# Optimization experiments

Measured on AMD Instinct MI355X. Metric: run time of the kernel, lower is better.

## Reference

```python
import jax, jax.numpy as jnp
import numpy as np

S, R, C, H, D = 128, 384, 256, 8, 32  # N_seq, N_res, C_m, heads, head_dim
INF = 1e9
EPS = 1e-5


def _layernorm(x, w, b):
    mu = jnp.mean(x, axis=-1, keepdims=True)
    var = jnp.mean(jnp.square(x - mu), axis=-1, keepdims=True)
    return (x - mu) * jax.lax.rsqrt(var + EPS) * w + b


def setup_inputs() -> dict:
    key = jax.random.key(0)
    ks = jax.random.split(key, 8)
    sc = 0.02
    m = jax.random.normal(ks[0], (S, R, C), jnp.float32)
    mask = jnp.ones((S, R), jnp.float32)
    ln_w = jnp.ones((C,), jnp.float32)
    ln_b = jnp.zeros((C,), jnp.float32)
    wq = jax.random.normal(ks[1], (C, H * D), jnp.float32) * sc
    wk = jax.random.normal(ks[2], (C, H * D), jnp.float32) * sc
    wv = jax.random.normal(ks[3], (C, H * D), jnp.float32) * sc
    wg = jax.random.normal(ks[4], (C, H * D), jnp.float32) * sc
    bg = jnp.ones((H * D,), jnp.float32)  # gate bias init to 1 (openfold convention)
    wo = jax.random.normal(ks[5], (H * D, C), jnp.float32) * sc
    bo = jnp.zeros((C,), jnp.float32)
    return {"m": m, "mask": mask, "ln_w": ln_w, "ln_b": ln_b,
            "wq": wq, "wk": wk, "wv": wv, "wg": wg, "bg": bg,
            "wo": wo, "bo": bo}


def reference(m, mask, ln_w, ln_b, wq, wk, wv, wg, bg, wo, bo):
    # mask bias: [S, 1, 1, R], 0 where mask==1, -inf-ish where mask==0
    mask_bias = (INF * (mask - 1.0))[:, None, None, :]
    x = _layernorm(m, ln_w, ln_b)                        # [S, R, C]
    q = (x @ wq).reshape(S, R, H, D) * (D ** -0.5)       # [S, R, H, D]
    k = (x @ wk).reshape(S, R, H, D)
    v = (x @ wv).reshape(S, R, H, D)
    scores = jnp.einsum('sqhd,skhd->shqk', q, k) + mask_bias  # [S, H, R, R]
    a = jax.nn.softmax(scores, axis=-1)
    o = jnp.einsum('shqk,skhd->sqhd', a, v)              # [S, R, H, D]
    g = jax.nn.sigmoid(x @ wg + bg).reshape(S, R, H, D)  # gate
    o = (o * g).reshape(S, R, H * D)
    return o @ wo + bo                                   # [S, R, C]
```

## Files before the change

kernel.cpp:

```cpp
#include <hip/hip_runtime.h>
#include <cstdint>
#include <cstddef>

#define S_  128
#define R_  384
#define C_  256
#define H_  8
#define D_  32
#define HD_ 256
#define M_  (S_*R_)

#define LOG2E 1.4426950408889634f

typedef float f32x16 __attribute__((ext_vector_type(16)));
typedef short s16x8  __attribute__((ext_vector_type(8)));
typedef int   i32x4  __attribute__((ext_vector_type(4)));

__device__ __forceinline__ unsigned short f2bf(float f) {
  uint32_t u = __float_as_uint(f);
  u += 0x7fffu + ((u >> 16) & 1u);
  return (unsigned short)(u >> 16);
}
__device__ __forceinline__ float bf2f(unsigned short s) {
  return __uint_as_float(((uint32_t)s) << 16);
}
__device__ __forceinline__ uint32_t pkbf(float lo, float hi) {
  return (uint32_t)f2bf(lo) | ((uint32_t)f2bf(hi) << 16);
}
#define MFMA32(a,b,c) __builtin_amdgcn_mfma_f32_32x32x16_bf16((a),(b),(c),0,0,0)

__device__ __forceinline__ void gload16(const void* g, void* l) {
  __builtin_amdgcn_global_load_lds(
      (const __attribute__((address_space(1))) void*)g,
      (__attribute__((address_space(3))) void*)l, 16, 0, 0);
}

__global__ __launch_bounds__(256) void prep_w(const float* __restrict__ wq,
    const float* __restrict__ wk, const float* __restrict__ wv,
    const float* __restrict__ wg, const float* __restrict__ wo,
    unsigned short* __restrict__ WT) {
  __shared__ unsigned short Tl[64][72];
  const int mat = blockIdx.x >> 4;
  const int t   = blockIdx.x & 15;
  const int k0  = (t >> 2) * 64, n0 = (t & 3) * 64;
  const float* W = (mat==0)?wq:(mat==1)?wk:(mat==2)?wv:(mat==3)?wg:wo;
  const int tx = threadIdx.x & 63, ty = threadIdx.x >> 6;
#pragma unroll
  for (int i = 0; i < 16; i++) {
    int kk = ty + i * 4;
    Tl[tx][kk] = f2bf(W[(size_t)(k0 + kk) * 256 + n0 + tx]);
  }
  __syncthreads();
#pragma unroll
  for (int i = 0; i < 16; i++) {
    int nn = ty + i * 4;
    WT[(size_t)mat * 65536 + (size_t)(n0 + nn) * 256 + k0 + tx] = Tl[nn][tx];
  }
}

__global__ __launch_bounds__(256) void ln_kernel(const float* __restrict__ mIn,
    const float* __restrict__ w, const float* __restrict__ b,
    unsigned short* __restrict__ x) {
  int row  = blockIdx.x * 4 + (threadIdx.x >> 6);
  int lane = threadIdx.x & 63;
  const float4 v4 = *(const float4*)(mIn + (size_t)row * C_ + lane * 4);
  float s  = v4.x + v4.y + v4.z + v4.w;
  float ss = v4.x*v4.x + v4.y*v4.y + v4.z*v4.z + v4.w*v4.w;
#pragma unroll
  for (int off = 32; off > 0; off >>= 1) {
    s  += __shfl_xor(s,  off);
    ss += __shfl_xor(ss, off);
  }
  float mu  = s * (1.0f / C_);
  float var = ss * (1.0f / C_) - mu * mu;
  float rs  = rsqrtf(var + 1e-5f);
  const float4 wv = *(const float4*)(w + lane * 4);
  const float4 bv = *(const float4*)(b + lane * 4);
  uint2 o2;
  o2.x = pkbf((v4.x - mu) * rs * wv.x + bv.x, (v4.y - mu) * rs * wv.y + bv.y);
  o2.y = pkbf((v4.z - mu) * rs * wv.z + bv.z, (v4.w - mu) * rs * wv.w + bv.w);
  *(uint2*)(x + (size_t)row * C_ + lane * 4) = o2;
}

__global__ __launch_bounds__(256, 5) void proj_gemm(const unsigned short* __restrict__ X,
    const unsigned short* __restrict__ WT, const float* __restrict__ bg,
    unsigned short* __restrict__ Qo, unsigned short* __restrict__ Ko,
    unsigned short* __restrict__ Vo, unsigned short* __restrict__ Go) {
  __shared__ __align__(16) unsigned short As[64 * 32];
  __shared__ __align__(16) unsigned short Bs[128 * 32];
  const int tid = threadIdx.x;
  const int wi  = blockIdx.x >> 1;
  const int bn  = (blockIdx.x & 1) * 128;
  const int bm  = blockIdx.y * 64;
  const unsigned short* Wt = WT + (size_t)wi * 65536;
  unsigned short* O = (wi==0)?Qo:(wi==1)?Ko:(wi==2)?Vo:Go;

  const int lane = tid & 63, wid = tid >> 6;
  const int wr = (wid >> 1) * 32, wc = (wid & 1) * 64;
  const int lr = lane & 31, hi = lane >> 5;
  const int srow = lane >> 2, scol = (lane & 3) * 8;

  f32x16 acc0, acc1;
#pragma unroll
  for (int r = 0; r < 16; r++) { acc0[r] = 0.f; acc1[r] = 0.f; }

  for (int k0 = 0; k0 < 256; k0 += 32) {
    gload16(X + (size_t)(bm + wid*16 + srow) * 256 + k0 + scol, &As[wid * 512]);
#pragma unroll
    for (int i = 0; i < 2; i++) {
      const int rb = wid * 32 + i * 16;
      gload16(Wt + (size_t)(bn + rb + srow) * 256 + k0 + scol, &Bs[rb * 32]);
    }
    asm volatile("s_waitcnt vmcnt(0)" ::: "memory");
    __syncthreads();
#pragma unroll
    for (int kh = 0; kh < 2; kh++) {
      s16x8 a0 = *(const s16x8*)&As[(wr + lr) * 32      + kh*16 + 8*hi];
      s16x8 b0 = *(const s16x8*)&Bs[(wc + lr) * 32      + kh*16 + 8*hi];
      s16x8 b1 = *(const s16x8*)&Bs[(wc + 32 + lr) * 32 + kh*16 + 8*hi];
      acc0 = MFMA32(a0, b0, acc0);
      acc1 = MFMA32(a0, b1, acc1);
    }
    __syncthreads();
  }

  const float qs2 = 0.17677669529663687f * LOG2E;
#pragma unroll
  for (int ns = 0; ns < 2; ns++) {
    const f32x16& a = ns ? acc1 : acc0;
    int colg = bn + wc + ns*32 + lr;
    float bgv = (wi == 3) ? bg[colg] : 0.f;
#pragma unroll
    for (int r = 0; r < 16; r++) {
      float v = a[r];
      if (wi == 0) v *= qs2;
      if (wi == 3) v = 1.0f / (1.0f + __expf(-(v + bgv)));
      int row = bm + wr + (r & 3) + 8*(r >> 2) + 4*hi;
      O[(size_t)row * 256 + colg] = f2bf(v);
    }
  }
}

__global__ __launch_bounds__(768, 6) void attn_kernel(const unsigned short* __restrict__ Qb,
    const unsigned short* __restrict__ Kb, const unsigned short* __restrict__ Vb,
    const unsigned short* __restrict__ Gb, const float* __restrict__ mask,
    unsigned short* __restrict__ Ob) {
  __shared__ unsigned short Kl[384][40];
  __shared__ unsigned short VT[32][392];
  __shared__ float mb[384];
  __shared__ float sAl[12][32];

  const int h = blockIdx.x, s = blockIdx.y;
  const int tid = threadIdx.x;
  const int wid = tid >> 6, lane = tid & 63;
  const int lr = lane & 31, hi = lane >> 5;

  if (tid < 384) {
    const unsigned short* ksrc = Kb + ((size_t)(s*R_ + tid)) * 256 + h*32;
    uint4 k0 = *(const uint4*)ksrc;
    uint4 k1 = *(const uint4*)(ksrc + 8);
    uint4 k2 = *(const uint4*)(ksrc + 16);
    uint4 k3 = *(const uint4*)(ksrc + 24);
    *(uint4*)&Kl[tid][0]  = k0;
    *(uint4*)&Kl[tid][8]  = k1;
    *(uint4*)&Kl[tid][16] = k2;
    *(uint4*)&Kl[tid][24] = k3;
    mb[tid] = (1e9f * LOG2E) * (mask[s * R_ + tid] - 1.0f);
  } else {
    const int r = tid - 384;
    const unsigned short* vsrc = Vb + ((size_t)(s*R_ + r)) * 256 + h*32;
    unsigned short tmp[32];
    *(uint4*)(tmp)      = *(const uint4*)vsrc;
    *(uint4*)(tmp + 8)  = *(const uint4*)(vsrc + 8);
    *(uint4*)(tmp + 16) = *(const uint4*)(vsrc + 16);
    *(uint4*)(tmp + 24) = *(const uint4*)(vsrc + 24);
#pragma unroll
    for (int j = 0; j < 32; j++) VT[j][r] = tmp[j];
  }

  const int q0 = wid * 32;
  const unsigned short* qsrc = Qb + ((size_t)(s*R_ + q0 + lr)) * 256 + h*32;
  s16x8 bq0 = *(const s16x8*)(qsrc + 8*hi);
  s16x8 bq1 = *(const s16x8*)(qsrc + 16 + 8*hi);

  f32x16 of;
#pragma unroll
  for (int r = 0; r < 16; r++) of[r] = 0.f;
  float mrun = -1e30f, lsum = 0.f;

  __syncthreads();

  for (int kt = 0; kt < 12; kt++) {
    s16x8 ak0 = *(const s16x8*)&Kl[kt*32 + lr][8*hi];
    s16x8 ak1 = *(const s16x8*)&Kl[kt*32 + lr][16 + 8*hi];
    s16x8 bv0 = *(const s16x8*)&VT[lr][kt*32 + 8*hi];
    s16x8 bv1 = *(const s16x8*)&VT[lr][kt*32 + 16 + 8*hi];

    f32x16 p;
#pragma unroll
    for (int r = 0; r < 16; r++) p[r] = mb[kt*32 + (r & 3) + 8*(r >> 2) + 4*hi];
    __builtin_amdgcn_s_setprio(1);
    p = MFMA32(ak0, bq0, p);
    p = MFMA32(ak1, bq1, p);
    __builtin_amdgcn_s_setprio(0);

    float m01 = fmaxf(fmaxf(p[0], p[1]), fmaxf(p[2], p[3]));
    float m23 = fmaxf(fmaxf(p[4], p[5]), fmaxf(p[6], p[7]));
    float m45 = fmaxf(fmaxf(p[8], p[9]), fmaxf(p[10], p[11]));
    float m67 = fmaxf(fmaxf(p[12], p[13]), fmaxf(p[14], p[15]));
    float pm = fmaxf(fmaxf(m01, m23), fmaxf(m45, m67));
    pm = fmaxf(pm, __shfl_xor(pm, 32));
    if (!__all(pm <= mrun + 11.54f)) {
      float nm = fmaxf(mrun, pm);
      float al = __builtin_amdgcn_exp2f(mrun - nm);
      mrun = nm;
      lsum *= al;
      if (hi == 0) sAl[wid][lr] = al;
#pragma unroll
      for (int r = 0; r < 16; r++)
        of[r] *= sAl[wid][(r & 3) + 8*(r >> 2) + 4*hi];
    }
    float ls = 0.f;
#pragma unroll
    for (int r = 0; r < 16; r++) {
      p[r] = __builtin_amdgcn_exp2f(p[r] - mrun);
      ls += p[r];
    }
    lsum += ls;

    uint32_t w0, w1, w2, w3, w4, w5, w6, w7;
    asm("v_cvt_pk_bf16_f32 %0, %1, %2" : "=v"(w0) : "v"(p[0]),  "v"(p[1]));
    asm("v_cvt_pk_bf16_f32 %0, %1, %2" : "=v"(w1) : "v"(p[2]),  "v"(p[3]));
    asm("v_cvt_pk_bf16_f32 %0, %1, %2" : "=v"(w2) : "v"(p[4]),  "v"(p[5]));
    asm("v_cvt_pk_bf16_f32 %0, %1, %2" : "=v"(w3) : "v"(p[6]),  "v"(p[7]));
    asm("v_cvt_pk_bf16_f32 %0, %1, %2" : "=v"(w4) : "v"(p[8]),  "v"(p[9]));
    asm("v_cvt_pk_bf16_f32 %0, %1, %2" : "=v"(w5) : "v"(p[10]), "v"(p[11]));
    asm("v_cvt_pk_bf16_f32 %0, %1, %2" : "=v"(w6) : "v"(p[12]), "v"(p[13]));
    asm("v_cvt_pk_bf16_f32 %0, %1, %2" : "=v"(w7) : "v"(p[14]), "v"(p[15]));
    asm volatile("v_permlane32_swap_b32 %0, %1" : "+v"(w0), "+v"(w2));
    asm volatile("v_permlane32_swap_b32 %0, %1" : "+v"(w1), "+v"(w3));
    asm volatile("v_permlane32_swap_b32 %0, %1" : "+v"(w4), "+v"(w6));
    asm volatile("v_permlane32_swap_b32 %0, %1" : "+v"(w5), "+v"(w7));
    i32x4 pa0i = {(int)w0, (int)w1, (int)w2, (int)w3};
    i32x4 pa1i = {(int)w4, (int)w5, (int)w6, (int)w7};
    __builtin_amdgcn_s_setprio(1);
    of = MFMA32(__builtin_bit_cast(s16x8, pa0i), bv0, of);
    of = MFMA32(__builtin_bit_cast(s16x8, pa1i), bv1, of);
    __builtin_amdgcn_s_setprio(0);
  }

  float lt = lsum + __shfl_xor(lsum, 32);
  float inv = 1.0f / lt;
  if (hi == 0) sAl[wid][lr] = inv;
#pragma unroll
  for (int r = 0; r < 16; r++) {
    int crow = (r & 3) + 8*(r >> 2) + 4*hi;
    float iv = sAl[wid][crow];
    size_t off = ((size_t)(s*R_ + q0 + crow)) * 256 + h*32 + lr;
    float gv = bf2f(Gb[off]);
    Ob[off] = f2bf(of[r] * iv * gv);
  }
}

__global__ __launch_bounds__(256, 5) void out_gemm(const unsigned short* __restrict__ Ob,
    const unsigned short* __restrict__ WT, const float* __restrict__ bo,
    float* __restrict__ Out) {
  __shared__ __align__(16) unsigned short As[64 * 32];
  __shared__ __align__(16) unsigned short Bs[128 * 32];
  const unsigned short* Wt = WT + 4 * 65536;
  const int tid = threadIdx.x;
  const int bn = blockIdx.x * 128;
  const int bm = blockIdx.y * 64;
  const int lane = tid & 63, wid = tid >> 6;
  const int wr = (wid >> 1) * 32, wc = (wid & 1) * 64;
  const int lr = lane & 31, hi = lane >> 5;
  const int srow = lane >> 2, scol = (lane & 3) * 8;

  f32x16 acc0, acc1;
#pragma unroll
  for (int r = 0; r < 16; r++) { acc0[r] = 0.f; acc1[r] = 0.f; }

  for (int k0 = 0; k0 < 256; k0 += 32) {
    gload16(Ob + (size_t)(bm + wid*16 + srow) * 256 + k0 + scol, &As[wid * 512]);
#pragma unroll
    for (int i = 0; i < 2; i++) {
      const int rb = wid * 32 + i * 16;
      gload16(Wt + (size_t)(bn + rb + srow) * 256 + k0 + scol, &Bs[rb * 32]);
    }
    asm volatile("s_waitcnt vmcnt(0)" ::: "memory");
    __syncthreads();
#pragma unroll
    for (int kh = 0; kh < 2; kh++) {
      s16x8 a0 = *(const s16x8*)&As[(wr + lr) * 32      + kh*16 + 8*hi];
      s16x8 b0 = *(const s16x8*)&Bs[(wc + lr) * 32      + kh*16 + 8*hi];
      s16x8 b1 = *(const s16x8*)&Bs[(wc + 32 + lr) * 32 + kh*16 + 8*hi];
      acc0 = MFMA32(a0, b0, acc0);
      acc1 = MFMA32(a0, b1, acc1);
    }
    __syncthreads();
  }

#pragma unroll
  for (int ns = 0; ns < 2; ns++) {
    const f32x16& a = ns ? acc1 : acc0;
    int colg = bn + wc + ns*32 + lr;
    float bov = bo[colg];
#pragma unroll
    for (int r = 0; r < 16; r++) {
      int row = bm + wr + (r & 3) + 8*(r >> 2) + 4*hi;
      Out[(size_t)row * 256 + colg] = a[r] + bov;
    }
  }
}

extern "C" void kernel_launch(void* const* d_in, const int* in_sizes, int n_in,
                              void* d_out, int out_size, void* d_ws, size_t ws_size,
                              hipStream_t stream) {
  const float* m    = (const float*)d_in[0];
  const float* mask = (const float*)d_in[1];
  const float* ln_w = (const float*)d_in[2];
  const float* ln_b = (const float*)d_in[3];
  const float* wq   = (const float*)d_in[4];
  const float* wk   = (const float*)d_in[5];
  const float* wv   = (const float*)d_in[6];
  const float* wg   = (const float*)d_in[7];
  const float* bg   = (const float*)d_in[8];
  const float* wo   = (const float*)d_in[9];
  const float* bo   = (const float*)d_in[10];
  float* out = (float*)d_out;

  unsigned short* ws = (unsigned short*)d_ws;
  const size_t SZ = (size_t)M_ * 256;
  unsigned short* xbf = ws;
  unsigned short* qb  = ws + 1 * SZ;
  unsigned short* kb  = ws + 2 * SZ;
  unsigned short* vb  = ws + 3 * SZ;
  unsigned short* gb  = ws + 4 * SZ;
  unsigned short* ob  = ws + 5 * SZ;
  unsigned short* WT  = ws + 6 * SZ;

  prep_w<<<80, 256, 0, stream>>>(wq, wk, wv, wg, wo, WT);
  ln_kernel<<<M_ / 4, 256, 0, stream>>>(m, ln_w, ln_b, xbf);
  proj_gemm<<<dim3(8, M_ / 64), 256, 0, stream>>>(xbf, WT, bg, qb, kb, vb, gb);
  attn_kernel<<<dim3(H_, S_), 768, 0, stream>>>(qb, kb, vb, gb, mask, ob);
  out_gemm<<<dim3(2, M_ / 64), 256, 0, stream>>>(ob, WT, bo, out);
}
```

Measured before the change: 241.4 us.

## Double-buffer LDS tiles in projection and output GEMMs to overlap loads

Both bf16 GEMM kernels now keep two LDS buffers and prefetch the next K-slice with direct global-to-LDS loads while MFMAs consume the current one. Partial vmcnt waits and explicit s_barrier fences wrapped in scheduling barriers replace the old full wait plus __syncthreads. The goal is to hide global-load latency in the K loop. In exchange LDS per block doubles and the occupancy hint of 5 blocks per CU is dropped, which may lower occupancy.

Result: slower. 246.8 us (+2.2%).

```diff
diff --git a/kernel.cpp b/kernel.cpp
--- a/kernel.cpp
+++ b/kernel.cpp
@@ -33,6 +33,12 @@
   __builtin_amdgcn_global_load_lds(
       (const __attribute__((address_space(1))) void*)g,
       (__attribute__((address_space(3))) void*)l, 16, 0, 0);
+}
+
+__device__ __forceinline__ void barrier_fence() {
+  __builtin_amdgcn_sched_barrier(0);
+  asm volatile("s_barrier" ::: "memory");
+  __builtin_amdgcn_sched_barrier(0);
 }
 
 __global__ __launch_bounds__(256) void prep_w(const float* __restrict__ wq,
@@ -82,12 +88,12 @@
   *(uint2*)(x + (size_t)row * C_ + lane * 4) = o2;
 }
 
-__global__ __launch_bounds__(256, 5) void proj_gemm(const unsigned short* __restrict__ X,
+__global__ __launch_bounds__(256) void proj_gemm(const unsigned short* __restrict__ X,
     const unsigned short* __restrict__ WT, const float* __restrict__ bg,
     unsigned short* __restrict__ Qo, unsigned short* __restrict__ Ko,
     unsigned short* __restrict__ Vo, unsigned short* __restrict__ Go) {
-  __shared__ __align__(16) unsigned short As[64 * 32];
-  __shared__ __align__(16) unsigned short Bs[128 * 32];
+  __shared__ __align__(16) unsigned short As[2][64 * 32];
+  __shared__ __align__(16) unsigned short Bs[2][128 * 32];
   const int tid = threadIdx.x;
   const int wi  = blockIdx.x >> 1;
   const int bn  = (blockIdx.x & 1) * 128;
@@ -100,29 +106,43 @@
   const int lr = lane & 31, hi = lane >> 5;
   const int srow = lane >> 2, scol = (lane & 3) * 8;
 
+  const unsigned short* Xs = X  + (size_t)(bm + wid*16 + srow) * 256 + scol;
+  const unsigned short* W0 = Wt + (size_t)(bn + wid*32 + srow) * 256 + scol;
+  const unsigned short* W1 = W0 + 16 * 256;
+
+#define PSTAGE(buf, k0) do {                         \
+    gload16(Xs + (k0), &As[buf][wid * 512]);          \
+    gload16(W0 + (k0), &Bs[buf][(wid*32) * 32]);      \
+    gload16(W1 + (k0), &Bs[buf][(wid*32 + 16) * 32]); \
+  } while (0)
+
   f32x16 acc0, acc1;
 #pragma unroll
   for (int r = 0; r < 16; r++) { acc0[r] = 0.f; acc1[r] = 0.f; }
 
-  for (int k0 = 0; k0 < 256; k0 += 32) {
-    gload16(X + (size_t)(bm + wid*16 + srow) * 256 + k0 + scol, &As[wid * 512]);
-#pragma unroll
-    for (int i = 0; i < 2; i++) {
-      const int rb = wid * 32 + i * 16;
-      gload16(Wt + (size_t)(bn + rb + srow) * 256 + k0 + scol, &Bs[rb * 32]);
-    }
-    asm volatile("s_waitcnt vmcnt(0)" ::: "memory");
-    __syncthreads();
+  PSTAGE(0, 0);
+#pragma unroll
+  for (int t = 0; t < 8; ++t) {
+    if (t < 7) {
+      PSTAGE((t + 1) & 1, (t + 1) * 32);
+      asm volatile("s_waitcnt vmcnt(3)" ::: "memory");
+    } else {
+      asm volatile("s_waitcnt vmcnt(0)" ::: "memory");
+    }
+    barrier_fence();
+    const unsigned short* Ab = As[t & 1];
+    const unsigned short* Bb = Bs[t & 1];
 #pragma unroll
     for (int kh = 0; kh < 2; kh++) {
-      s16x8 a0 = *(const s16x8*)&As[(wr + lr) * 32      + kh*16 + 8*hi];
-      s16x8 b0 = *(const s16x8*)&Bs[(wc + lr) * 32      + kh*16 + 8*hi];
-      s16x8 b1 = *(const s16x8*)&Bs[(wc + 32 + lr) * 32 + kh*16 + 8*hi];
+      s16x8 a0 = *(const s16x8*)&Ab[(wr + lr) * 32      + kh*16 + 8*hi];
+      s16x8 b0 = *(const s16x8*)&Bb[(wc + lr) * 32      + kh*16 + 8*hi];
+      s16x8 b1 = *(const s16x8*)&Bb[(wc + 32 + lr) * 32 + kh*16 + 8*hi];
       acc0 = MFMA32(a0, b0, acc0);
       acc1 = MFMA32(a0, b1, acc1);
     }
-    __syncthreads();
-  }
+    barrier_fence();
+  }
+#undef PSTAGE
 
   const float qs2 = 0.17677669529663687f * LOG2E;
 #pragma unroll
@@ -262,11 +282,11 @@
   }
 }
 
-__global__ __launch_bounds__(256, 5) void out_gemm(const unsigned short* __restrict__ Ob,
+__global__ __launch_bounds__(256) void out_gemm(const unsigned short* __restrict__ Ob,
     const unsigned short* __restrict__ WT, const float* __restrict__ bo,
     float* __restrict__ Out) {
-  __shared__ __align__(16) unsigned short As[64 * 32];
-  __shared__ __align__(16) unsigned short Bs[128 * 32];
+  __shared__ __align__(16) unsigned short As[2][64 * 32];
+  __shared__ __align__(16) unsigned short Bs[2][128 * 32];
   const unsigned short* Wt = WT + 4 * 65536;
   const int tid = threadIdx.x;
   const int bn = blockIdx.x * 128;
@@ -276,29 +296,43 @@
   const int lr = lane & 31, hi = lane >> 5;
   const int srow = lane >> 2, scol = (lane & 3) * 8;
 
+  const unsigned short* Asrc = Ob + (size_t)(bm + wid*16 + srow) * 256 + scol;
+  const unsigned short* W0   = Wt + (size_t)(bn + wid*32 + srow) * 256 + scol;
+  const unsigned short* W1   = W0 + 16 * 256;
+
+#define OSTAGE(buf, k0) do {                          \
+    gload16(Asrc + (k0), &As[buf][wid * 512]);         \
+    gload16(W0   + (k0), &Bs[buf][(wid*32) * 32]);     \
+    gload16(W1   + (k0), &Bs[buf][(wid*32 + 16) * 32]);\
+  } while (0)
+
   f32x16 acc0, acc1;
 #pragma unroll
   for (int r = 0; r < 16; r++) { acc0[r] = 0.f; acc1[r] = 0.f; }
 
-  for (int k0 = 0; k0 < 256; k0 += 32) {
-    gload16(Ob + (size_t)(bm + wid*16 + srow) * 256 + k0 + scol, &As[wid * 512]);
-#pragma unroll
-    for (int i = 0; i < 2; i++) {
-      const int rb = wid * 32 + i * 16;
-      gload16(Wt + (size_t)(bn + rb + srow) * 256 + k0 + scol, &Bs[rb * 32]);
-    }
-    asm volatile("s_waitcnt vmcnt(0)" ::: "memory");
-    __syncthreads();
+  OSTAGE(0, 0);
+#pragma unroll
+  for (int t = 0; t < 8; ++t) {
+    if (t < 7) {
+      OSTAGE((t + 1) & 1, (t + 1) * 32);
+      asm volatile("s_waitcnt vmcnt(3)" ::: "memory");
+    } else {
+      asm volatile("s_waitcnt vmcnt(0)" ::: "memory");
+    }
+    barrier_fence();
+    const unsigned short* Ab = As[t & 1];
+    const unsigned short* Bb = Bs[t & 1];
 #pragma unroll
     for (int kh = 0; kh < 2; kh++) {
-      s16x8 a0 = *(const s16x8*)&As[(wr + lr) * 32      + kh*16 + 8*hi];
-      s16x8 b0 = *(const s16x8*)&Bs[(wc + lr) * 32      + kh*16 + 8*hi];
-      s16x8 b1 = *(const s16x8*)&Bs[(wc + 32 + lr) * 32 + kh*16 + 8*hi];
+      s16x8 a0 = *(const s16x8*)&Ab[(wr + lr) * 32      + kh*16 + 8*hi];
+      s16x8 b0 = *(const s16x8*)&Bb[(wc + lr) * 32      + kh*16 + 8*hi];
+      s16x8 b1 = *(const s16x8*)&Bb[(wc + 32 + lr) * 32 + kh*16 + 8*hi];
       acc0 = MFMA32(a0, b0, acc0);
       acc1 = MFMA32(a0, b1, acc1);
     }
-    __syncthreads();
-  }
+    barrier_fence();
+  }
+#undef OSTAGE
 
 #pragma unroll
   for (int ns = 0; ns < 2; ns++) {
```

## Enlarge GEMM tiles to 128x128, swizzle block order, merge weight-prep with layernorm

Applied to the files above, without the earlier changes.

The projection and output GEMMs move from 64x128 to 128x128 block tiles, with each wave computing a 2x2 grid of 32x32 MFMA tiles. This raises operand reuse per LDS load and halves the number of blocks. A block-index remap spreads consecutive blocks across the 8 XCD-style groups so neighbouring blocks share rows and weights. The weight transpose and layernorm kernels are fused into one launch to save a kernel launch. The price is more accumulator registers, fewer blocks for latency hiding, and dropping the occupancy hint from the launch bounds.

After: 230.4 us. -4.6%, faster.

```diff
diff --git a/kernel.cpp b/kernel.cpp
--- a/kernel.cpp
+++ b/kernel.cpp
@@ -35,108 +35,120 @@
       (__attribute__((address_space(3))) void*)l, 16, 0, 0);
 }
 
-__global__ __launch_bounds__(256) void prep_w(const float* __restrict__ wq,
+__global__ __launch_bounds__(256) void prep_ln(const float* __restrict__ wq,
     const float* __restrict__ wk, const float* __restrict__ wv,
     const float* __restrict__ wg, const float* __restrict__ wo,
-    unsigned short* __restrict__ WT) {
+    const float* __restrict__ mIn, const float* __restrict__ lw,
+    const float* __restrict__ lb,
+    unsigned short* __restrict__ WT, unsigned short* __restrict__ x) {
   __shared__ unsigned short Tl[64][72];
-  const int mat = blockIdx.x >> 4;
-  const int t   = blockIdx.x & 15;
-  const int k0  = (t >> 2) * 64, n0 = (t & 3) * 64;
-  const float* W = (mat==0)?wq:(mat==1)?wk:(mat==2)?wv:(mat==3)?wg:wo;
-  const int tx = threadIdx.x & 63, ty = threadIdx.x >> 6;
-#pragma unroll
-  for (int i = 0; i < 16; i++) {
-    int kk = ty + i * 4;
-    Tl[tx][kk] = f2bf(W[(size_t)(k0 + kk) * 256 + n0 + tx]);
-  }
-  __syncthreads();
-#pragma unroll
-  for (int i = 0; i < 16; i++) {
-    int nn = ty + i * 4;
-    WT[(size_t)mat * 65536 + (size_t)(n0 + nn) * 256 + k0 + tx] = Tl[nn][tx];
-  }
-}
-
-__global__ __launch_bounds__(256) void ln_kernel(const float* __restrict__ mIn,
-    const float* __restrict__ w, const float* __restrict__ b,
-    unsigned short* __restrict__ x) {
-  int row  = blockIdx.x * 4 + (threadIdx.x >> 6);
-  int lane = threadIdx.x & 63;
-  const float4 v4 = *(const float4*)(mIn + (size_t)row * C_ + lane * 4);
-  float s  = v4.x + v4.y + v4.z + v4.w;
-  float ss = v4.x*v4.x + v4.y*v4.y + v4.z*v4.z + v4.w*v4.w;
-#pragma unroll
-  for (int off = 32; off > 0; off >>= 1) {
-    s  += __shfl_xor(s,  off);
-    ss += __shfl_xor(ss, off);
-  }
-  float mu  = s * (1.0f / C_);
-  float var = ss * (1.0f / C_) - mu * mu;
-  float rs  = rsqrtf(var + 1e-5f);
-  const float4 wv = *(const float4*)(w + lane * 4);
-  const float4 bv = *(const float4*)(b + lane * 4);
-  uint2 o2;
-  o2.x = pkbf((v4.x - mu) * rs * wv.x + bv.x, (v4.y - mu) * rs * wv.y + bv.y);
-  o2.y = pkbf((v4.z - mu) * rs * wv.z + bv.z, (v4.w - mu) * rs * wv.w + bv.w);
-  *(uint2*)(x + (size_t)row * C_ + lane * 4) = o2;
-}
-
-__global__ __launch_bounds__(256, 5) void proj_gemm(const unsigned short* __restrict__ X,
+  if (blockIdx.x < 80) {
+    const int mat = blockIdx.x >> 4;
+    const int t   = blockIdx.x & 15;
+    const int k0  = (t >> 2) * 64, n0 = (t & 3) * 64;
+    const float* W = (mat==0)?wq:(mat==1)?wk:(mat==2)?wv:(mat==3)?wg:wo;
+    const int tx = threadIdx.x & 63, ty = threadIdx.x >> 6;
+#pragma unroll
+    for (int i = 0; i < 16; i++) {
+      int kk = ty + i * 4;
+      Tl[tx][kk] = f2bf(W[(size_t)(k0 + kk) * 256 + n0 + tx]);
+    }
+    __syncthreads();
+#pragma unroll
+    for (int i = 0; i < 16; i++) {
+      int nn = ty + i * 4;
+      WT[(size_t)mat * 65536 + (size_t)(n0 + nn) * 256 + k0 + tx] = Tl[nn][tx];
+    }
+  } else {
+    int row  = (blockIdx.x - 80) * 4 + (threadIdx.x >> 6);
+    int lane = threadIdx.x & 63;
+    const float4 v4 = *(const float4*)(mIn + (size_t)row * C_ + lane * 4);
+    float s  = v4.x + v4.y + v4.z + v4.w;
+    float ss = v4.x*v4.x + v4.y*v4.y + v4.z*v4.z + v4.w*v4.w;
+#pragma unroll
+    for (int off = 32; off > 0; off >>= 1) {
+      s  += __shfl_xor(s,  off);
+      ss += __shfl_xor(ss, off);
+    }
+    float mu  = s * (1.0f / C_);
+    float var = ss * (1.0f / C_) - mu * mu;
+    float rs  = rsqrtf(var + 1e-5f);
+    const float4 wv4 = *(const float4*)(lw + lane * 4);
+    const float4 bv4 = *(const float4*)(lb + lane * 4);
+    uint2 o2;
+    o2.x = pkbf((v4.x - mu) * rs * wv4.x + bv4.x, (v4.y - mu) * rs * wv4.y + bv4.y);
+    o2.y = pkbf((v4.z - mu) * rs * wv4.z + bv4.z, (v4.w - mu) * rs * wv4.w + bv4.w);
+    *(uint2*)(x + (size_t)row * C_ + lane * 4) = o2;
+  }
+}
+
+__global__ __launch_bounds__(256) void proj_gemm(const unsigned short* __restrict__ X,
     const unsigned short* __restrict__ WT, const float* __restrict__ bg,
     unsigned short* __restrict__ Qo, unsigned short* __restrict__ Ko,
     unsigned short* __restrict__ Vo, unsigned short* __restrict__ Go) {
-  __shared__ __align__(16) unsigned short As[64 * 32];
+  __shared__ __align__(16) unsigned short As[128 * 32];
   __shared__ __align__(16) unsigned short Bs[128 * 32];
-  const int tid = threadIdx.x;
-  const int wi  = blockIdx.x >> 1;
-  const int bn  = (blockIdx.x & 1) * 128;
-  const int bm  = blockIdx.y * 64;
+  const int bid  = blockIdx.x;
+  const int sbid = (bid & 7) * 384 + (bid >> 3);
+  const int wsel = sbid & 7;
+  const int bm   = (sbid >> 3) * 128;
+  const int wi   = wsel >> 1;
+  const int bn   = (wsel & 1) * 128;
   const unsigned short* Wt = WT + (size_t)wi * 65536;
   unsigned short* O = (wi==0)?Qo:(wi==1)?Ko:(wi==2)?Vo:Go;
 
+  const int tid = threadIdx.x;
   const int lane = tid & 63, wid = tid >> 6;
-  const int wr = (wid >> 1) * 32, wc = (wid & 1) * 64;
+  const int wm = (wid >> 1) * 64, wn = (wid & 1) * 64;
   const int lr = lane & 31, hi = lane >> 5;
   const int srow = lane >> 2, scol = (lane & 3) * 8;
 
-  f32x16 acc0, acc1;
-#pragma unroll
-  for (int r = 0; r < 16; r++) { acc0[r] = 0.f; acc1[r] = 0.f; }
+  f32x16 acc[2][2];
+#pragma unroll
+  for (int i = 0; i < 2; i++)
+#pragma unroll
+    for (int j = 0; j < 2; j++)
+#pragma unroll
+      for (int r = 0; r < 16; r++) acc[i][j][r] = 0.f;
 
   for (int k0 = 0; k0 < 256; k0 += 32) {
-    gload16(X + (size_t)(bm + wid*16 + srow) * 256 + k0 + scol, &As[wid * 512]);
 #pragma unroll
     for (int i = 0; i < 2; i++) {
-      const int rb = wid * 32 + i * 16;
-      gload16(Wt + (size_t)(bn + rb + srow) * 256 + k0 + scol, &Bs[rb * 32]);
+      const int rbase = wid * 32 + i * 16;
+      gload16(X  + (size_t)(bm + rbase + srow) * 256 + k0 + scol, &As[rbase * 32]);
+      gload16(Wt + (size_t)(bn + rbase + srow) * 256 + k0 + scol, &Bs[rbase * 32]);
     }
     asm volatile("s_waitcnt vmcnt(0)" ::: "memory");
     __syncthreads();
 #pragma unroll
     for (int kh = 0; kh < 2; kh++) {
-      s16x8 a0 = *(const s16x8*)&As[(wr + lr) * 32      + kh*16 + 8*hi];
-      s16x8 b0 = *(const s16x8*)&Bs[(wc + lr) * 32      + kh*16 + 8*hi];
-      s16x8 b1 = *(const s16x8*)&Bs[(wc + 32 + lr) * 32 + kh*16 + 8*hi];
-      acc0 = MFMA32(a0, b0, acc0);
-      acc1 = MFMA32(a0, b1, acc1);
+      s16x8 a0 = *(const s16x8*)&As[(wm + lr) * 32      + kh*16 + 8*hi];
+      s16x8 a1 = *(const s16x8*)&As[(wm + 32 + lr) * 32 + kh*16 + 8*hi];
+      s16x8 b0 = *(const s16x8*)&Bs[(wn + lr) * 32      + kh*16 + 8*hi];
+      s16x8 b1 = *(const s16x8*)&Bs[(wn + 32 + lr) * 32 + kh*16 + 8*hi];
+      acc[0][0] = MFMA32(a0, b0, acc[0][0]);
+      acc[0][1] = MFMA32(a0, b1, acc[0][1]);
+      acc[1][0] = MFMA32(a1, b0, acc[1][0]);
+      acc[1][1] = MFMA32(a1, b1, acc[1][1]);
     }
     __syncthreads();
   }
 
   const float qs2 = 0.17677669529663687f * LOG2E;
 #pragma unroll
-  for (int ns = 0; ns < 2; ns++) {
-    const f32x16& a = ns ? acc1 : acc0;
-    int colg = bn + wc + ns*32 + lr;
-    float bgv = (wi == 3) ? bg[colg] : 0.f;
-#pragma unroll
-    for (int r = 0; r < 16; r++) {
-      float v = a[r];
-      if (wi == 0) v *= qs2;
-      if (wi == 3) v = 1.0f / (1.0f + __expf(-(v + bgv)));
-      int row = bm + wr + (r & 3) + 8*(r >> 2) + 4*hi;
-      O[(size_t)row * 256 + colg] = f2bf(v);
+  for (int ms = 0; ms < 2; ms++) {
+#pragma unroll
+    for (int ns = 0; ns < 2; ns++) {
+      int colg = bn + wn + ns*32 + lr;
+      float bgv = (wi == 3) ? bg[colg] : 0.f;
+#pragma unroll
+      for (int r = 0; r < 16; r++) {
+        float v = acc[ms][ns][r];
+        if (wi == 0) v *= qs2;
+        if (wi == 3) v = 1.0f / (1.0f + __expf(-(v + bgv)));
+        int row = bm + wm + ms*32 + (r & 3) + 8*(r >> 2) + 4*hi;
+        O[(size_t)row * 256 + colg] = f2bf(v);
+      }
     }
   }
 }
@@ -262,53 +274,64 @@
   }
 }
 
-__global__ __launch_bounds__(256, 5) void out_gemm(const unsigned short* __restrict__ Ob,
+__global__ __launch_bounds__(256) void out_gemm(const unsigned short* __restrict__ Ob,
     const unsigned short* __restrict__ WT, const float* __restrict__ bo,
     float* __restrict__ Out) {
-  __shared__ __align__(16) unsigned short As[64 * 32];
+  __shared__ __align__(16) unsigned short As[128 * 32];
   __shared__ __align__(16) unsigned short Bs[128 * 32];
   const unsigned short* Wt = WT + 4 * 65536;
+  const int bid  = blockIdx.x;
+  const int sbid = (bid & 7) * 96 + (bid >> 3);
+  const int bn   = (sbid & 1) * 128;
+  const int bm   = (sbid >> 1) * 128;
   const int tid = threadIdx.x;
-  const int bn = blockIdx.x * 128;
-  const int bm = blockIdx.y * 64;
   const int lane = tid & 63, wid = tid >> 6;
-  const int wr = (wid >> 1) * 32, wc = (wid & 1) * 64;
+  const int wm = (wid >> 1) * 64, wn = (wid & 1) * 64;
   const int lr = lane & 31, hi = lane >> 5;
   const int srow = lane >> 2, scol = (lane & 3) * 8;
 
-  f32x16 acc0, acc1;
-#pragma unroll
-  for (int r = 0; r < 16; r++) { acc0[r] = 0.f; acc1[r] = 0.f; }
+  f32x16 acc[2][2];
+#pragma unroll
+  for (int i = 0; i < 2; i++)
+#pragma unroll
+    for (int j = 0; j < 2; j++)
+#pragma unroll
+      for (int r = 0; r < 16; r++) acc[i][j][r] = 0.f;
 
   for (int k0 = 0; k0 < 256; k0 += 32) {
-    gload16(Ob + (size_t)(bm + wid*16 + srow) * 256 + k0 + scol, &As[wid * 512]);
 #pragma unroll
     for (int i = 0; i < 2; i++) {
-      const int rb = wid * 32 + i * 16;
-      gload16(Wt + (size_t)(bn + rb + srow) * 256 + k0 + scol, &Bs[rb * 32]);
+      const int rbase = wid * 32 + i * 16;
+      gload16(Ob + (size_t)(bm + rbase + srow) * 256 + k0 + scol, &As[rbase * 32]);
+      gload16(Wt + (size_t)(bn + rbase + srow) * 256 + k0 + scol, &Bs[rbase * 32]);
     }
     asm volatile("s_waitcnt vmcnt(0)" ::: "memory");
     __syncthreads();
 #pragma unroll
     for (int kh = 0; kh < 2; kh++) {
-      s16x8 a0 = *(const s16x8*)&As[(wr + lr) * 32      + kh*16 + 8*hi];
-      s16x8 b0 = *(const s16x8*)&Bs[(wc + lr) * 32      + kh*16 + 8*hi];
-      s16x8 b1 = *(const s16x8*)&Bs[(wc + 32 + lr) * 32 + kh*16 + 8*hi];
-      acc0 = MFMA32(a0, b0, acc0);
-      acc1 = MFMA32(a0, b1, acc1);
-    }
-    __syncthreads();
-  }
-
-#pragma unroll
-  for (int ns = 0; ns < 2; ns++) {
-    const f32x16& a = ns ? acc1 : acc0;
-    int colg = bn + wc + ns*32 + lr;
-    float bov = bo[colg];
-#pragma unroll
-    for (int r = 0; r < 16; r++) {
-      int row = bm + wr + (r & 3) + 8*(r >> 2) + 4*hi;
-      Out[(size_t)row * 256 + colg] = a[r] + bov;
+      s16x8 a0 = *(const s16x8*)&As[(wm + lr) * 32      + kh*16 + 8*hi];
+      s16x8 a1 = *(const s16x8*)&As[(wm + 32 + lr) * 32 + kh*16 + 8*hi];
+      s16x8 b0 = *(const s16x8*)&Bs[(wn + lr) * 32      + kh*16 + 8*hi];
+      s16x8 b1 = *(const s16x8*)&Bs[(wn + 32 + lr) * 32 + kh*16 + 8*hi];
+      acc[0][0] = MFMA32(a0, b0, acc[0][0]);
+      acc[0][1] = MFMA32(a0, b1, acc[0][1]);
+      acc[1][0] = MFMA32(a1, b0, acc[1][0]);
+      acc[1][1] = MFMA32(a1, b1, acc[1][1]);
+    }
+    __syncthreads();
+  }
+
+#pragma unroll
+  for (int ms = 0; ms < 2; ms++) {
+#pragma unroll
+    for (int ns = 0; ns < 2; ns++) {
+      int colg = bn + wn + ns*32 + lr;
+      float bov = bo[colg];
+#pragma unroll
+      for (int r = 0; r < 16; r++) {
+        int row = bm + wm + ms*32 + (r & 3) + 8*(r >> 2) + 4*hi;
+        Out[(size_t)row * 256 + colg] = acc[ms][ns][r] + bov;
+      }
     }
   }
 }
@@ -339,9 +362,9 @@
   unsigned short* ob  = ws + 5 * SZ;
   unsigned short* WT  = ws + 6 * SZ;
 
-  prep_w<<<80, 256, 0, stream>>>(wq, wk, wv, wg, wo, WT);
-  ln_kernel<<<M_ / 4, 256, 0, stream>>>(m, ln_w, ln_b, xbf);
-  proj_gemm<<<dim3(8, M_ / 64), 256, 0, stream>>>(xbf, WT, bg, qb, kb, vb, gb);
+  prep_ln<<<80 + M_ / 4, 256, 0, stream>>>(wq, wk, wv, wg, wo, m, ln_w, ln_b,
+                                           WT, xbf);
+  proj_gemm<<<3072, 256, 0, stream>>>(xbf, WT, bg, qb, kb, vb, gb);
   attn_kernel<<<dim3(H_, S_), 768, 0, stream>>>(qb, kb, vb, gb, mask, ob);
-  out_gemm<<<dim3(2, M_ / 64), 256, 0, stream>>>(ob, WT, bo, out);
-}
+  out_gemm<<<768, 256, 0, stream>>>(ob, WT, bo, out);
+}
```
